# Optimization experiments

Hardware: AMD Instinct MI355X
Metric: run time of the kernel (lower is better)

Reference implementation:

```python
import jax, jax.numpy as jnp
from jax import lax
import numpy as np

B, DIM, L_IN = 8, 512, 4096
SCALE = 2
KSIZE = 17
DN = ('NCH', 'OIH', 'NCH')  # conv1d dimension numbers


def _aa_kernel(kernel_size: int, scale: int) -> np.ndarray:
    # replicates scipy.signal.kaiser_atten / kaiser_beta / windows.kaiser
    atten = 2.285 * (kernel_size - 1) * np.pi * (1.0 / scale) + 7.95
    if atten > 50:
        beta = 0.1102 * (atten - 8.7)
    elif atten > 21:
        beta = 0.5842 * (atten - 21) ** 0.4 + 0.07886 * (atten - 21)
    else:
        beta = 0.0
    win = np.kaiser(kernel_size, beta)
    xk = np.arange(kernel_size) - kernel_size // 2
    k = np.sinc(xk / scale) * win  # normalized sinc, same as torch.sinc
    return (k / k.sum()).astype(np.float32)


def setup_inputs() -> dict:
    key = jax.random.key(0)
    k1, k2, k3, k4, k5 = jax.random.split(key, 5)
    kconv = 2 * SCALE - 1
    return {
        'x': jax.random.normal(k1, (B, DIM, L_IN), dtype=jnp.float32),
        'conv_w': jax.random.normal(k2, (DIM, DIM, kconv), dtype=jnp.float32) * (1.0 / np.sqrt(DIM * kconv)),
        'conv_b': jax.random.normal(k3, (DIM,), dtype=jnp.float32) * 0.01,
        'aa_kernel': jnp.asarray(_aa_kernel(KSIZE, SCALE)),
        'proj_w': jax.random.normal(k4, (DIM, DIM), dtype=jnp.float32) * (1.0 / np.sqrt(DIM)),
        'proj_b': jax.random.normal(k5, (DIM,), dtype=jnp.float32) * 0.01,
    }


def reference(x, conv_w, conv_b, aa_kernel, proj_w, proj_b):
    s = SCALE
    # zero-insertion upsample + Conv1d(dim,dim,2s-1,pad=s-1) fused via lhs_dilation.
    # Torch zero-inserts to length l*s (trailing s-1 zeros), so right pad is 2s-2.
    y = lax.conv_general_dilated(
        x, conv_w, window_strides=(1,), padding=[(s - 1, 2 * s - 2)],
        lhs_dilation=(s,), dimension_numbers=DN,
    ) + conv_b[None, :, None]  # [B, D, l*s]
    # depthwise anti-alias filter (same Kaiser-sinc kernel per channel)
    dw = jnp.broadcast_to(aa_kernel, (DIM, 1, KSIZE))
    y = lax.conv_general_dilated(
        y, dw, window_strides=(1,), padding=[(KSIZE // 2, KSIZE // 2)],
        feature_group_count=DIM, dimension_numbers=DN,
    )
    # pointwise 1x1 projection
    return jnp.einsum('bdl,ed->bel', y, proj_w) + proj_b[None, :, None]
```

## Files before the change

kernel.cpp:

```cpp
#include <hip/hip_runtime.h>
#include <hip/hip_bf16.h>

#define BB_   8
#define DIM_  512
#define LIN_  4096
#define LOUT_ 8192

typedef __attribute__((ext_vector_type(8))) __bf16 bf16x8;
typedef __attribute__((ext_vector_type(4))) float  f32x4;
typedef __attribute__((ext_vector_type(8))) unsigned short u16x8;

__device__ __forceinline__ float bf2f(unsigned short u) {
  union { unsigned int i; float f; } x;
  x.i = ((unsigned int)u) << 16;
  return x.f;
}

__global__ __launch_bounds__(256) void k_prep(const float* __restrict__ proj_w,
                                              const float* __restrict__ conv_w,
                                              const float* __restrict__ conv_b,
                                              __hip_bfloat16* __restrict__ Mst,
                                              float* __restrict__ Pcb) {
  __shared__ float smem[2 * 32 * 33];
  const int bx  = blockIdx.x;
  const int tid = threadIdx.x;
  if (bx < 768) {
    const int kk = bx >> 8;
    const int et = ((bx >> 4) & 15) * 32;
    const int it = (bx & 15) * 32;
    float* Pt = smem;
    float* Wt = smem + 32 * 33;
    const int tx = tid & 15, ty = tid >> 4;
    float acc[2][2] = {};
    for (int d0 = 0; d0 < DIM_; d0 += 32) {
      {
        const int i = tid >> 3;
        const int j = (tid & 7) * 4;
        const float4 v = *(const float4*)&proj_w[(size_t)(et + i) * DIM_ + d0 + j];
        Pt[i * 33 + j] = v.x; Pt[i * 33 + j + 1] = v.y;
        Pt[i * 33 + j + 2] = v.z; Pt[i * 33 + j + 3] = v.w;
      }
#pragma unroll
      for (int r2 = 0; r2 < 4; ++r2) {
        const int id2 = tid + r2 * 256;
        const int i = id2 >> 5, j = id2 & 31;
        Wt[i * 33 + j] = conv_w[(size_t)(d0 + i) * (DIM_ * 3) + (it + j) * 3 + kk];
      }
      __syncthreads();
#pragma unroll
      for (int dl = 0; dl < 32; ++dl) {
        float pv[2], wv[2];
        pv[0] = Pt[(ty * 2) * 33 + dl];     pv[1] = Pt[(ty * 2 + 1) * 33 + dl];
        wv[0] = Wt[dl * 33 + tx * 2];       wv[1] = Wt[dl * 33 + tx * 2 + 1];
#pragma unroll
        for (int a = 0; a < 2; ++a)
#pragma unroll
          for (int bq = 0; bq < 2; ++bq) acc[a][bq] += pv[a] * wv[bq];
      }
      __syncthreads();
    }
#pragma unroll
    for (int a = 0; a < 2; ++a)
#pragma unroll
      for (int bq = 0; bq < 2; ++bq)
        Mst[(size_t)(kk * DIM_ + et + ty * 2 + a) * DIM_ + it + tx * 2 + bq] =
            __float2bfloat16(acc[a][bq]);
  } else {
    const int idx = bx - 768;
    const int e = idx * 4 + (tid >> 6);
    const int j = tid & 63;
    float s = 0.f;
#pragma unroll
    for (int d = j; d < DIM_; d += 64) s += proj_w[(size_t)e * DIM_ + d] * conv_b[d];
#pragma unroll
    for (int off = 32; off > 0; off >>= 1) s += __shfl_down(s, off, 64);
    if (j == 0) Pcb[e] = s;
  }
}

__global__ __launch_bounds__(256, 2) void k_gemm(const float* __restrict__ x,
                                                 const __hip_bfloat16* __restrict__ Mst,
                                                 const float* __restrict__ Pcb,
                                                 __hip_bfloat16* __restrict__ U) {
  __shared__ __align__(16) __hip_bfloat16 Bs[64 * 512];
  __shared__ __align__(16) __hip_bfloat16 As[2][128 * 32];
  const int tid = threadIdx.x;
  const int ct = blockIdx.x;
  const int bb = ct >> 6;
  const int l0 = (ct & 63) * 64;

  {
    const float* xb = x + (size_t)bb * DIM_ * LIN_ + l0;
    const int dr = tid >> 4;
    const int lc = (tid & 15) * 4;
#pragma unroll 4
    for (int p = 0; p < 32; ++p) {
      const int d = p * 16 + dr;
      const float4 v = *(const float4*)(xb + (size_t)d * LIN_ + lc);
      const int c8 = d >> 3, d7 = d & 7;
      const float vv[4] = {v.x, v.y, v.z, v.w};
#pragma unroll
      for (int j = 0; j < 4; ++j) {
        const int l = lc + j;
        Bs[l * 512 + ((c8 ^ (l & 7)) << 3) + d7] = __float2bfloat16(vv[j]);
      }
    }
  }

  const int r   = tid >> 2;
  const int chA = tid & 3;
  const int swz = chA ^ (r & 3);
  bf16x8 gA0 = *(const bf16x8*)(Mst + (size_t)r * 512 + swz * 8);
  bf16x8 gA1 = *(const bf16x8*)(Mst + (size_t)(r + 64) * 512 + swz * 8);
  *(bf16x8*)(&As[0][r * 32 + chA * 8]) = gA0;
  *(bf16x8*)(&As[0][(r + 64) * 32 + chA * 8]) = gA1;
  __syncthreads();

  const int lane = tid & 63;
  const int wave = tid >> 6;
  const int wm = wave >> 1, wn = wave & 1;
  const int kq = lane >> 4;
  const int mrow = wm * 64 + (lane & 15);
  const int slotA = kq ^ (lane & 3);
  const int lcol0 = wn * 32 + (lane & 15);

  f32x4 acc[4][2] = {};

  for (int it = 0; it < 192; ++it) {
    const int rt = it >> 4, kt = it & 15;
    const int cur = it & 1, nxt = cur ^ 1;

    if (it < 191) {
      const int itn = it + 1;
      const int rtn = itn >> 4, ktn = itn & 15;
      const __hip_bfloat16* ap =
          Mst + (size_t)(rtn * 128 + r) * 512 + ktn * 32 + swz * 8;
      gA0 = *(const bf16x8*)(ap);
      gA1 = *(const bf16x8*)(ap + (size_t)64 * 512);
    }

    bf16x8 af[4], bfr[2];
#pragma unroll
    for (int mt = 0; mt < 4; ++mt)
      af[mt] = *(const bf16x8*)(&As[cur][(mrow + mt * 16) * 32 + slotA * 8]);
    const int ck = kt * 4 + kq;
#pragma unroll
    for (int nt = 0; nt < 2; ++nt) {
      const int l = lcol0 + nt * 16;
      bfr[nt] = *(const bf16x8*)(&Bs[l * 512 + ((ck ^ (lane & 7)) << 3)]);
    }
#pragma unroll
    for (int mt = 0; mt < 4; ++mt)
#pragma unroll
      for (int nt = 0; nt < 2; ++nt)
        acc[mt][nt] = __builtin_amdgcn_mfma_f32_16x16x32_bf16(af[mt], bfr[nt],
                                                              acc[mt][nt], 0, 0, 0);

    if (it < 191) {
      *(bf16x8*)(&As[nxt][r * 32 + chA * 8]) = gA0;
      *(bf16x8*)(&As[nxt][(r + 64) * 32 + chA * 8]) = gA1;
    }

    if (kt == 15) {
      const int kk = rt >> 2;
      const int e0 = (rt & 3) * 128 + wm * 64;
#pragma unroll
      for (int mt = 0; mt < 4; ++mt) {
#pragma unroll
        for (int nt = 0; nt < 2; ++nt) {
          const int l = l0 + wn * 32 + nt * 16 + (lane & 15);
          const int ebase = e0 + mt * 16 + kq * 4;
#pragma unroll
          for (int rr = 0; rr < 4; ++rr) {
            float v = acc[mt][nt][rr];
            const int e = ebase + rr;
            if (kk < 2) v += Pcb[e];
            U[(size_t)((kk * 8 + bb) * 512 + e) * 4096 + l] = __float2bfloat16(v);
            acc[mt][nt][rr] = 0.f;
          }
        }
      }
    }
    __syncthreads();
  }
}

__global__ __launch_bounds__(256) void k_aa(const __hip_bfloat16* __restrict__ U,
                                            const float* __restrict__ aa,
                                            const float* __restrict__ proj_b,
                                            float* __restrict__ out) {
  const int b  = blockIdx.x >> 9;
  const int e  = blockIdx.x & 511;
  const int l0 = blockIdx.y << 11;
  const int tid = threadIdx.x;
  const int lt = l0 + 8 * tid;
  const unsigned short* q0 = (const unsigned short*)(U + (size_t)((0 * 8 + b) * 512 + e) * 4096);
  const unsigned short* q1 = (const unsigned short*)(U + (size_t)((1 * 8 + b) * 512 + e) * 4096);
  const unsigned short* q2 = (const unsigned short*)(U + (size_t)((2 * 8 + b) * 512 + e) * 4096);

  float E[17], O[16];
  if (lt >= 8 && lt + 16 <= 4096) {
    const int base = lt - 8;
    unsigned short r1[24], r0[24], r2[24];
#pragma unroll
    for (int c = 0; c < 3; ++c) {
      const u16x8 a = *(const u16x8*)(q1 + base + 8 * c);
      const u16x8 d = *(const u16x8*)(q0 + base + 8 * c);
      const u16x8 g = *(const u16x8*)(q2 + base + 8 * c);
#pragma unroll
      for (int j = 0; j < 8; ++j) {
        r1[8 * c + j] = a[j]; r0[8 * c + j] = d[j]; r2[8 * c + j] = g[j];
      }
    }
#pragma unroll
    for (int j = 0; j < 17; ++j) E[j] = bf2f(r1[4 + j]);
#pragma unroll
    for (int j = 0; j < 16; ++j) O[j] = bf2f(r0[4 + j]) + bf2f(r2[5 + j]);
  } else {
#pragma unroll
    for (int j = 0; j < 17; ++j) {
      const int l = lt - 4 + j;
      E[j] = (l >= 0 && l < 4096) ? bf2f(q1[l]) : 0.f;
    }
#pragma unroll
    for (int j = 0; j < 16; ++j) {
      const int l = lt - 4 + j;
      float v = 0.f;
      if (l >= 0 && l < 4096) {
        v = bf2f(q0[l]);
        if (l + 1 < 4096) v += bf2f(q2[l + 1]);
      }
      O[j] = v;
    }
  }

  float sa[17];
#pragma unroll
  for (int j = 0; j < 17; ++j) sa[j] = aa[j];
  const float pb = proj_b[e];
  float res[16];
#pragma unroll
  for (int t = 0; t < 8; ++t) {
    float se = 0.f, so = 0.f;
#pragma unroll
    for (int q = 0; q <= 8; ++q) {
      se += sa[2 * q] * E[t + q];
      so += sa[2 * q] * O[t + q];
    }
#pragma unroll
    for (int q = 0; q < 8; ++q) {
      se += sa[2 * q + 1] * O[t + q];
      so += sa[2 * q + 1] * E[t + q + 1];
    }
    res[2 * t]     = se + pb;
    res[2 * t + 1] = so + pb;
  }
  float* orow = out + (size_t)(b * 512 + e) * 8192 + 2 * lt;
#pragma unroll
  for (int c = 0; c < 4; ++c)
    *(float4*)(orow + 4 * c) = *(const float4*)&res[4 * c];
}

extern "C" void kernel_launch(void* const* d_in, const int* in_sizes, int n_in,
                              void* d_out, int out_size, void* d_ws, size_t ws_size,
                              hipStream_t stream) {
  const float* x      = (const float*)d_in[0];
  const float* conv_w = (const float*)d_in[1];
  const float* conv_b = (const float*)d_in[2];
  const float* aa     = (const float*)d_in[3];
  const float* proj_w = (const float*)d_in[4];
  const float* proj_b = (const float*)d_in[5];
  float* out = (float*)d_out;

  char* ws = (char*)d_ws;
  __hip_bfloat16* Mst = (__hip_bfloat16*)ws;
  float*          Pcb = (float*)(ws + 1572864);
  __hip_bfloat16* U   = (__hip_bfloat16*)(ws + 1576960);

  k_prep<<<dim3(896, 1, 1), 256, 0, stream>>>(proj_w, conv_w, conv_b, Mst, Pcb);
  k_gemm<<<dim3(512, 1, 1), 256, 0, stream>>>(x, Mst, Pcb, U);
  k_aa<<<dim3(4096, 2), 256, 0, stream>>>(U, aa, proj_b, out);
}
```

Measured before the change: 370.3 us.

## Pre-transpose x to bf16 and retile GEMM with 256x256 tiles and async LDS loads

The prep kernel now also converts x into a transposed bf16 layout [B, L, D], and the weight-product tiles are enlarged to 64x64 with a 4x4 register block. The GEMM is restructured so each 512-thread block computes a 256x256 output tile. It streams A and B through a 4-deep LDS ring using global_load_lds with explicit vmcnt waits, and remaps block IDs across XCDs. The aim is more data reuse per tile, fewer LDS passes for the x conversion, and latency hidden by the pipeline. The cost is an extra 32 MB workspace round trip for Xbt and heavy register pressure from 32 accumulators per thread.

```diff
diff --git a/kernel.cpp b/kernel.cpp
--- a/kernel.cpp
+++ b/kernel.cpp
@@ -16,57 +16,74 @@
   return x.f;
 }
 
+__device__ __forceinline__ unsigned short f2bf(float f) {
+  unsigned int u = __float_as_uint(f);
+  return (unsigned short)((u + 0x7fffu + ((u >> 16) & 1u)) >> 16);
+}
+
+__device__ __forceinline__ void gload16(const void* g, void* l) {
+  __builtin_amdgcn_global_load_lds(
+      (__attribute__((address_space(1))) void*)(g),
+      (__attribute__((address_space(3))) void*)(l), 16, 0, 0);
+}
+
 __global__ __launch_bounds__(256) void k_prep(const float* __restrict__ proj_w,
                                               const float* __restrict__ conv_w,
                                               const float* __restrict__ conv_b,
-                                              __hip_bfloat16* __restrict__ Mst,
-                                              float* __restrict__ Pcb) {
-  __shared__ float smem[2 * 32 * 33];
+                                              const float* __restrict__ x,
+                                              unsigned short* __restrict__ Mst,
+                                              float* __restrict__ Pcb,
+                                              unsigned short* __restrict__ Xbt) {
+  __shared__ __align__(16) float sm[4160];
   const int bx  = blockIdx.x;
   const int tid = threadIdx.x;
-  if (bx < 768) {
-    const int kk = bx >> 8;
-    const int et = ((bx >> 4) & 15) * 32;
-    const int it = (bx & 15) * 32;
-    float* Pt = smem;
-    float* Wt = smem + 32 * 33;
+
+  if (bx < 192) {
+    float* Pt = sm;
+    float* Wt = sm + 1088;
+    const int kk = bx >> 6;
+    const int t6 = bx & 63;
+    const int et = (t6 >> 3) << 6;
+    const int it = (t6 & 7) << 6;
     const int tx = tid & 15, ty = tid >> 4;
-    float acc[2][2] = {};
-    for (int d0 = 0; d0 < DIM_; d0 += 32) {
+    const int le = tid & 63, lg = tid >> 6;
+    float acc[4][4] = {};
+    for (int d0 = 0; d0 < DIM_; d0 += 16) {
       {
-        const int i = tid >> 3;
-        const int j = (tid & 7) * 4;
-        const float4 v = *(const float4*)&proj_w[(size_t)(et + i) * DIM_ + d0 + j];
-        Pt[i * 33 + j] = v.x; Pt[i * 33 + j + 1] = v.y;
-        Pt[i * 33 + j + 2] = v.z; Pt[i * 33 + j + 3] = v.w;
-      }
-#pragma unroll
-      for (int r2 = 0; r2 < 4; ++r2) {
-        const int id2 = tid + r2 * 256;
-        const int i = id2 >> 5, j = id2 & 31;
-        Wt[i * 33 + j] = conv_w[(size_t)(d0 + i) * (DIM_ * 3) + (it + j) * 3 + kk];
+        const float4 v = *(const float4*)&proj_w[(size_t)(et + le) * DIM_ + d0 + lg * 4];
+        Pt[(lg * 4 + 0) * 68 + le] = v.x;
+        Pt[(lg * 4 + 1) * 68 + le] = v.y;
+        Pt[(lg * 4 + 2) * 68 + le] = v.z;
+        Pt[(lg * 4 + 3) * 68 + le] = v.w;
+      }
+#pragma unroll
+      for (int r = 0; r < 4; ++r) {
+        const int dl = r * 4 + lg;
+        Wt[dl * 68 + le] = conv_w[(size_t)(d0 + dl) * (DIM_ * 3) + (it + le) * 3 + kk];
       }
       __syncthreads();
 #pragma unroll
-      for (int dl = 0; dl < 32; ++dl) {
-        float pv[2], wv[2];
-        pv[0] = Pt[(ty * 2) * 33 + dl];     pv[1] = Pt[(ty * 2 + 1) * 33 + dl];
-        wv[0] = Wt[dl * 33 + tx * 2];       wv[1] = Wt[dl * 33 + tx * 2 + 1];
-#pragma unroll
-        for (int a = 0; a < 2; ++a)
-#pragma unroll
-          for (int bq = 0; bq < 2; ++bq) acc[a][bq] += pv[a] * wv[bq];
+      for (int dl = 0; dl < 16; ++dl) {
+        const float4 pv = *(const float4*)&Pt[dl * 68 + ty * 4];
+        const float4 wv = *(const float4*)&Wt[dl * 68 + tx * 4];
+        const float pa[4] = {pv.x, pv.y, pv.z, pv.w};
+        const float wa[4] = {wv.x, wv.y, wv.z, wv.w};
+#pragma unroll
+        for (int a = 0; a < 4; ++a)
+#pragma unroll
+          for (int b = 0; b < 4; ++b) acc[a][b] += pa[a] * wa[b];
       }
       __syncthreads();
     }
 #pragma unroll
-    for (int a = 0; a < 2; ++a)
-#pragma unroll
-      for (int bq = 0; bq < 2; ++bq)
-        Mst[(size_t)(kk * DIM_ + et + ty * 2 + a) * DIM_ + it + tx * 2 + bq] =
-            __float2bfloat16(acc[a][bq]);
-  } else {
-    const int idx = bx - 768;
+    for (int a = 0; a < 4; ++a) {
+      uint2 pk;
+      pk.x = (unsigned int)f2bf(acc[a][0]) | ((unsigned int)f2bf(acc[a][1]) << 16);
+      pk.y = (unsigned int)f2bf(acc[a][2]) | ((unsigned int)f2bf(acc[a][3]) << 16);
+      *(uint2*)&Mst[(size_t)(kk * DIM_ + et + ty * 4 + a) * DIM_ + it + tx * 4] = pk;
+    }
+  } else if (bx < 320) {
+    const int idx = bx - 192;
     const int e = idx * 4 + (tid >> 6);
     const int j = tid & 63;
     float s = 0.f;
@@ -75,113 +92,130 @@
 #pragma unroll
     for (int off = 32; off > 0; off >>= 1) s += __shfl_down(s, off, 64);
     if (j == 0) Pcb[e] = s;
-  }
-}
-
-__global__ __launch_bounds__(256, 2) void k_gemm(const float* __restrict__ x,
-                                                 const __hip_bfloat16* __restrict__ Mst,
+  } else {
+    const int bc = bx - 320;
+    const int bb = bc >> 9;
+    const int dt = ((bc >> 6) & 7) << 6;
+    const int lt = (bc & 63) << 6;
+    const int lr  = tid >> 4;
+    const int lc4 = (tid & 15) << 2;
+#pragma unroll
+    for (int r = 0; r < 4; ++r) {
+      const int d = r * 16 + lr;
+      const float4 v = *(const float4*)&x[((size_t)(bb * DIM_ + dt + d) << 12) + lt + lc4];
+      float* row = sm + d * 65 + lc4;
+      row[0] = v.x; row[1] = v.y; row[2] = v.z; row[3] = v.w;
+    }
+    __syncthreads();
+#pragma unroll
+    for (int rr = 0; rr < 2; ++rr) {
+      const int flat = rr * 256 + tid;
+      const int l  = flat >> 3;
+      const int d8 = (flat & 7) << 3;
+      unsigned int w[4];
+#pragma unroll
+      for (int p = 0; p < 4; ++p) {
+        const float f0 = sm[(d8 + 2 * p + 0) * 65 + l];
+        const float f1 = sm[(d8 + 2 * p + 1) * 65 + l];
+        w[p] = (unsigned int)f2bf(f0) | ((unsigned int)f2bf(f1) << 16);
+      }
+      uint4 pk; pk.x = w[0]; pk.y = w[1]; pk.z = w[2]; pk.w = w[3];
+      *(uint4*)&Xbt[((size_t)(bb * LIN_ + lt + l) << 9) + dt + d8] = pk;
+    }
+  }
+}
+
+__global__ __launch_bounds__(512, 2) void k_gemm(const unsigned short* __restrict__ Xbt,
+                                                 const unsigned short* __restrict__ Mst,
                                                  const float* __restrict__ Pcb,
-                                                 __hip_bfloat16* __restrict__ U) {
-  __shared__ __align__(16) __hip_bfloat16 Bs[64 * 512];
-  __shared__ __align__(16) __hip_bfloat16 As[2][128 * 32];
+                                                 unsigned short* __restrict__ U) {
+  __shared__ __align__(16) char lds[131072];
   const int tid = threadIdx.x;
-  const int ct = blockIdx.x;
-  const int bb = ct >> 6;
-  const int l0 = (ct & 63) * 64;
-
-  {
-    const float* xb = x + (size_t)bb * DIM_ * LIN_ + l0;
-    const int dr = tid >> 4;
-    const int lc = (tid & 15) * 4;
-#pragma unroll 4
-    for (int p = 0; p < 32; ++p) {
-      const int d = p * 16 + dr;
-      const float4 v = *(const float4*)(xb + (size_t)d * LIN_ + lc);
-      const int c8 = d >> 3, d7 = d & 7;
-      const float vv[4] = {v.x, v.y, v.z, v.w};
-#pragma unroll
-      for (int j = 0; j < 4; ++j) {
-        const int l = lc + j;
-        Bs[l * 512 + ((c8 ^ (l & 7)) << 3) + d7] = __float2bfloat16(vv[j]);
-      }
-    }
-  }
-
-  const int r   = tid >> 2;
-  const int chA = tid & 3;
-  const int swz = chA ^ (r & 3);
-  bf16x8 gA0 = *(const bf16x8*)(Mst + (size_t)r * 512 + swz * 8);
-  bf16x8 gA1 = *(const bf16x8*)(Mst + (size_t)(r + 64) * 512 + swz * 8);
-  *(bf16x8*)(&As[0][r * 32 + chA * 8]) = gA0;
-  *(bf16x8*)(&As[0][(r + 64) * 32 + chA * 8]) = gA1;
-  __syncthreads();
+  const int bid = blockIdx.x;
+  const int wgs   = (bid & 7) * 96 + (bid >> 3);
+  const int ntile = wgs / 6;
+  const int mtile = wgs - ntile * 6;
+  const int bb = ntile >> 4;
+  const int l0 = (ntile & 15) << 8;
+  const int m0 = mtile << 8;
+
+  const int srow   = tid >> 2;
+  const int schunk = (tid & 3) ^ ((srow >> 1) & 3);
+  const unsigned short* Ag = Mst + (size_t)(m0 + srow) * 512 + schunk * 8;
+  const unsigned short* Bg = Xbt + ((size_t)(bb * LIN_ + l0 + srow) << 9) + schunk * 8;
+  char* ldsw = lds + (tid >> 6) * 1024;
+
+#define STAGE_(kt_, buf_)                          \
+  do {                                             \
+    const unsigned short* ga_ = Ag + (kt_) * 32;   \
+    const unsigned short* gb_ = Bg + (kt_) * 32;   \
+    char* la_ = ldsw + (buf_) * 32768;             \
+    gload16(ga_,         la_);                     \
+    gload16(ga_ + 65536, la_ + 8192);              \
+    gload16(gb_,         la_ + 16384);             \
+    gload16(gb_ + 65536, la_ + 24576);             \
+  } while (0)
 
   const int lane = tid & 63;
   const int wave = tid >> 6;
-  const int wm = wave >> 1, wn = wave & 1;
-  const int kq = lane >> 4;
-  const int mrow = wm * 64 + (lane & 15);
-  const int slotA = kq ^ (lane & 3);
-  const int lcol0 = wn * 32 + (lane & 15);
-
-  f32x4 acc[4][2] = {};
-
-  for (int it = 0; it < 192; ++it) {
-    const int rt = it >> 4, kt = it & 15;
-    const int cur = it & 1, nxt = cur ^ 1;
-
-    if (it < 191) {
-      const int itn = it + 1;
-      const int rtn = itn >> 4, ktn = itn & 15;
-      const __hip_bfloat16* ap =
-          Mst + (size_t)(rtn * 128 + r) * 512 + ktn * 32 + swz * 8;
-      gA0 = *(const bf16x8*)(ap);
-      gA1 = *(const bf16x8*)(ap + (size_t)64 * 512);
-    }
-
-    bf16x8 af[4], bfr[2];
-#pragma unroll
-    for (int mt = 0; mt < 4; ++mt)
-      af[mt] = *(const bf16x8*)(&As[cur][(mrow + mt * 16) * 32 + slotA * 8]);
-    const int ck = kt * 4 + kq;
-#pragma unroll
-    for (int nt = 0; nt < 2; ++nt) {
-      const int l = lcol0 + nt * 16;
-      bfr[nt] = *(const bf16x8*)(&Bs[l * 512 + ((ck ^ (lane & 7)) << 3)]);
-    }
-#pragma unroll
-    for (int mt = 0; mt < 4; ++mt)
-#pragma unroll
-      for (int nt = 0; nt < 2; ++nt)
-        acc[mt][nt] = __builtin_amdgcn_mfma_f32_16x16x32_bf16(af[mt], bfr[nt],
+  const int wm = wave >> 2;
+  const int wn = wave & 3;
+  const int lrow = lane & 15;
+  const int lc   = lane >> 4;
+  const int aslot = lc ^ ((lrow >> 1) & 3);
+  const char* ldsA0 = lds + ((wm * 128 + lrow) * 64 + aslot * 16);
+  const char* ldsB0 = lds + (16384 + (wn * 64 + lrow) * 64 + aslot * 16);
+
+  f32x4 acc[8][4] = {};
+
+  STAGE_(0, 0); STAGE_(1, 1); STAGE_(2, 2);
+
+#pragma unroll 4
+  for (int kt = 0; kt < 16; ++kt) {
+    if (kt < 13) STAGE_(kt + 3, (kt + 3) & 3);
+    if (kt < 13)       asm volatile("s_waitcnt vmcnt(12)" ::: "memory");
+    else if (kt == 13) asm volatile("s_waitcnt vmcnt(8)" ::: "memory");
+    else if (kt == 14) asm volatile("s_waitcnt vmcnt(4)" ::: "memory");
+    else               asm volatile("s_waitcnt vmcnt(0)" ::: "memory");
+    __builtin_amdgcn_s_barrier();
+    __builtin_amdgcn_sched_barrier(0);
+
+    const int bo = (kt & 3) * 32768;
+    bf16x8 af[8], bfr[4];
+#pragma unroll
+    for (int mt = 0; mt < 8; ++mt) af[mt] = *(const bf16x8*)(ldsA0 + bo + mt * 1024);
+#pragma unroll
+    for (int nt = 0; nt < 4; ++nt) bfr[nt] = *(const bf16x8*)(ldsB0 + bo + nt * 1024);
+#pragma unroll
+    for (int mt = 0; mt < 8; ++mt)
+#pragma unroll
+      for (int nt = 0; nt < 4; ++nt)
+        acc[mt][nt] = __builtin_amdgcn_mfma_f32_16x16x32_bf16(bfr[nt], af[mt],
                                                               acc[mt][nt], 0, 0, 0);
-
-    if (it < 191) {
-      *(bf16x8*)(&As[nxt][r * 32 + chA * 8]) = gA0;
-      *(bf16x8*)(&As[nxt][(r + 64) * 32 + chA * 8]) = gA1;
-    }
-
-    if (kt == 15) {
-      const int kk = rt >> 2;
-      const int e0 = (rt & 3) * 128 + wm * 64;
-#pragma unroll
-      for (int mt = 0; mt < 4; ++mt) {
-#pragma unroll
-        for (int nt = 0; nt < 2; ++nt) {
-          const int l = l0 + wn * 32 + nt * 16 + (lane & 15);
-          const int ebase = e0 + mt * 16 + kq * 4;
-#pragma unroll
-          for (int rr = 0; rr < 4; ++rr) {
-            float v = acc[mt][nt][rr];
-            const int e = ebase + rr;
-            if (kk < 2) v += Pcb[e];
-            U[(size_t)((kk * 8 + bb) * 512 + e) * 4096 + l] = __float2bfloat16(v);
-            acc[mt][nt][rr] = 0.f;
-          }
-        }
-      }
-    }
-    __syncthreads();
+    asm volatile("s_waitcnt lgkmcnt(0)" ::: "memory");
+    __builtin_amdgcn_sched_barrier(0);
+    __builtin_amdgcn_s_barrier();
+  }
+#undef STAGE_
+
+  const int es0 = m0 + wm * 128 + lrow;
+  const int lq  = l0 + wn * 64 + (lc << 2);
+#pragma unroll
+  for (int mt = 0; mt < 8; ++mt) {
+    const int es = es0 + mt * 16;
+    const int kk = es >> 9;
+    const int e  = es & 511;
+    const float bias = (kk < 2) ? Pcb[e] : 0.f;
+    unsigned short* urow = U + (((size_t)((kk * 8 + bb) * 512 + e)) << 12) + lq;
+#pragma unroll
+    for (int nt = 0; nt < 4; ++nt) {
+      uint2 pk;
+      pk.x = (unsigned int)f2bf(acc[mt][nt][0] + bias) |
+             ((unsigned int)f2bf(acc[mt][nt][1] + bias) << 16);
+      pk.y = (unsigned int)f2bf(acc[mt][nt][2] + bias) |
+             ((unsigned int)f2bf(acc[mt][nt][3] + bias) << 16);
+      *(uint2*)(urow + nt * 16) = pk;
+    }
   }
 }
 
@@ -273,11 +307,12 @@
   float* out = (float*)d_out;
 
   char* ws = (char*)d_ws;
-  __hip_bfloat16* Mst = (__hip_bfloat16*)ws;
+  unsigned short* Mst = (unsigned short*)ws;
   float*          Pcb = (float*)(ws + 1572864);
-  __hip_bfloat16* U   = (__hip_bfloat16*)(ws + 1576960);
-
-  k_prep<<<dim3(896, 1, 1), 256, 0, stream>>>(proj_w, conv_w, conv_b, Mst, Pcb);
-  k_gemm<<<dim3(512, 1, 1), 256, 0, stream>>>(x, Mst, Pcb, U);
-  k_aa<<<dim3(4096, 2), 256, 0, stream>>>(U, aa, proj_b, out);
-}
+  unsigned short* Xbt = (unsigned short*)(ws + 1574912);
+  unsigned short* U   = (unsigned short*)(ws + 35129344);
+
+  k_prep<<<dim3(4416, 1, 1), 256, 0, stream>>>(proj_w, conv_w, conv_b, x, Mst, Pcb, Xbt);
+  k_gemm<<<dim3(768, 1, 1), 512, 0, stream>>>(Xbt, Mst, Pcb, U);
+  k_aa<<<dim3(4096, 2), 256, 0, stream>>>((const __hip_bfloat16*)U, aa, proj_b, out);
+}
```

After: 344.3 us. 1.08x faster.
